# Optimization experiments

Hardware: AMD Instinct MI355X
Metric: run time of the kernel (lower is better)

The kernel has to match this reference:

```python
import jax, jax.numpy as jnp
import numpy as np

NUM_ITEMS = 50000
B = 512      # batch of (user, item) pairs
L = 50       # padded per-user item-list length
K = 20       # top_k: length of each context channel
H = 32       # hidden_dim
D = 32       # output_dim


def setup_inputs() -> dict:
    key = jax.random.key(0)
    ks = jax.random.split(key, 8)
    ctx = jax.random.normal(ks[0], (NUM_ITEMS, 10, K), dtype=jnp.float32)
    item_idxs = jax.random.randint(ks[1], (B,), 0, NUM_ITEMS)
    user_items = jax.random.randint(ks[2], (B, L), 0, NUM_ITEMS)
    user_lens = jax.random.randint(ks[3], (B,), 1, L + 1)  # ragged lengths in [1, L]
    W1 = jax.random.normal(ks[4], (5, 1, H), dtype=jnp.float32) * 0.1
    b1 = jnp.zeros((5, H), dtype=jnp.float32)
    W2 = jax.random.normal(ks[5], (5, H, D), dtype=jnp.float32) * 0.1
    b2 = jnp.zeros((5, D), dtype=jnp.float32)
    Wout = jax.random.normal(ks[6], (D, 1), dtype=jnp.float32) * 0.1
    bout = jnp.zeros((1,), dtype=jnp.float32)
    return dict(ctx=ctx, W1=W1, b1=b1, W2=W2, b2=b2, Wout=Wout, bout=bout,
                item_idxs=item_idxs, user_items=user_items, user_lens=user_lens)


def _item_rep(feat, W1, b1, W2, b2):
    """feat: [..., 10, K] context channels -> [..., 5*K, D] item representation.
    Channels (2c, 2c+1) go through com_{c+1}: a shared 1->H->D MLP applied to each
    scalar (unsqueeze(1) in the original), outputs of the two channels multiplied."""
    prefix = feat.shape[:-2]
    x = feat.reshape(prefix + (5, 2, K))                     # [..., 5, 2, K]
    w1 = W1[:, 0, :].reshape((5, 1, 1, H))                   # input_dim == 1
    h = jax.nn.relu(x[..., None] * w1 + b1.reshape((5, 1, 1, H)))   # [..., 5, 2, K, H]
    o = jnp.einsum('...cpkh,chd->...cpkd', h, W2) + b2.reshape((5, 1, 1, D))
    rep = o[..., 0, :, :] * o[..., 1, :, :]                  # [..., 5, K, D]
    return rep.reshape(prefix + (5 * K, D))


def reference(ctx, W1, b1, W2, b2, Wout, bout, item_idxs, user_items, user_lens):
    # Target-item representations: gather contexts then tiny MLPs. [B, 5K, D]
    item_rep = _item_rep(ctx[item_idxs], W1, b1, W2, b2)
    # Per-user item reps (padded ragged) and masked mean over the item list.
    u_rep = _item_rep(ctx[user_items], W1, b1, W2, b2)       # [B, L, 5K, D]
    mask = (jnp.arange(L)[None, :] < user_lens[:, None]).astype(u_rep.dtype)  # [B, L]
    u_mean = jnp.einsum('blnd,bl->bnd', u_rep, mask) / user_lens[:, None, None].astype(u_rep.dtype)
    inter = u_mean * item_rep                                # [B, 5K, D]
    pred = jax.nn.sigmoid(inter @ Wout + bout)               # [B, 5K, 1]
    return pred.reshape(B * 5 * K, 1)
```

## Files before the change

### kernel.cpp

```cpp
#include <hip/hip_runtime.h>
#include <math.h>

#define NITEMS 50000
#define BATCH  512
#define LLEN   50
#define KTOP   20
#define HDIM   32
#define DDIM   32
#define NCH    5
#define NSEG   33
#define NSCAL  200
#define NCELL  100
#define THRP   33
#define NWAVE  8

#define WS_THRS  0
#define WS_AB    (NCH*HDIM)
#define WS_ORDER 10720

__global__ __launch_bounds__(256) void cnn_setup(
        const float* __restrict__ W1, const float* __restrict__ b1,
        const float* __restrict__ W2, const float* __restrict__ b2,
        const int* __restrict__ user_lens,
        float* __restrict__ ws, int* __restrict__ order) {
    const int tid = threadIdx.x;

    if (blockIdx.x < NSEG) {
        __shared__ float sW1[NCH*HDIM], sB1[NCH*HDIM], sThr[NCH*HDIM];
        __shared__ int   sRank[NCH*HDIM];
        __shared__ float sW2[NCH*HDIM*DDIM];
        __shared__ float sB2[NCH*DDIM];

        for (int i = tid; i < NCH*HDIM; i += 256) { sW1[i] = W1[i]; sB1[i] = b1[i]; }
        for (int i = tid; i < NCH*HDIM*DDIM; i += 256) sW2[i] = W2[i];
        for (int i = tid; i < NCH*DDIM; i += 256) sB2[i] = b2[i];
        __syncthreads();

        for (int i = tid; i < NCH*HDIM; i += 256) {
            float w = sW1[i];
            sThr[i] = (w != 0.f) ? (-sB1[i] / w) : INFINITY;
        }
        __syncthreads();

        for (int i = tid; i < NCH*HDIM; i += 256) {
            int c = i / HDIM, h = i % HDIM;
            float thr = sThr[i];
            int rank = 0;
            for (int h2 = 0; h2 < HDIM; ++h2) {
                float thr2 = sThr[c*HDIM + h2];
                rank += (thr2 < thr || (thr2 == thr && h2 < h)) ? 1 : 0;
            }
            sRank[i] = rank;
            if (blockIdx.x == 0) ws[WS_THRS + c*HDIM + rank] = thr;
        }
        __syncthreads();

        const int s = blockIdx.x;
        if (tid < NCH*DDIM) {
            int c = tid / DDIM, d = tid % DDIM;
            float A = 0.f, Bv = 0.f;
#pragma unroll
            for (int h = 0; h < HDIM; ++h) {
                float w  = sW1[c*HDIM + h];
                float bb = sB1[c*HDIM + h];
                int   r  = sRank[c*HDIM + h];
                bool active = (w > 0.f) ? (r < s) : ((w < 0.f) ? (r >= s) : (bb > 0.f));
                if (active) {
                    float w2 = sW2[(c*HDIM + h)*DDIM + d];
                    A  = fmaf(w,  w2, A);
                    Bv = fmaf(bb, w2, Bv);
                }
            }
            Bv += sB2[c*DDIM + d];
            float* AB = ws + WS_AB;
            AB[((c*NSEG + s)*DDIM + d)*2 + 0] = A;
            AB[((c*NSEG + s)*DDIM + d)*2 + 1] = Bv;
        }
    } else {
        __shared__ int k512[BATCH], v512[BATCH];
        for (int i = tid; i < BATCH; i += 256) { k512[i] = user_lens[i]; v512[i] = i; }
        __syncthreads();
        for (int k = 2; k <= BATCH; k <<= 1) {
            for (int j = k >> 1; j > 0; j >>= 1) {
                int i   = ((tid & ~(j - 1)) << 1) | (tid & (j - 1));
                int ixj = i | j;
                bool up = ((i & k) == 0);
                int ka = k512[i], kb = k512[ixj];
                if ((ka > kb) == up) {
                    k512[i] = kb; k512[ixj] = ka;
                    int va = v512[i]; v512[i] = v512[ixj]; v512[ixj] = va;
                }
                __syncthreads();
            }
        }
        for (int i = tid; i < BATCH; i += 256) order[i] = v512[i];
    }
}

__global__ __launch_bounds__(512, 4) void cnn_main(
        const float* __restrict__ ctx,  const float* __restrict__ ws,
        const float* __restrict__ Wout, const float* __restrict__ bout,
        const int* __restrict__ item_idxs, const int* __restrict__ user_items,
        const int* __restrict__ user_lens, const int* __restrict__ order,
        float* __restrict__ out) {
    __shared__ float4 sAB4[NCH*NSEG*16];
    __shared__ float  sThrS[NCH*THRP];
    __shared__ float4 sxo[NWAVE][NCELL];
    __shared__ union WScr {
        float rawx[NSCAL];
        float pRed[NCELL];
    } wscr[NWAVE];

    const int tid  = threadIdx.x;
    const int w    = tid >> 6;
    const int lane = tid & 63;
    const int g    = (lane >> 4) & 3;
    const int d16  = lane & 15;

    const float4* ABg = reinterpret_cast<const float4*>(ws + WS_AB);
    for (int i = tid; i < NCH*NSEG*16; i += 512) sAB4[i] = ABg[i];
    for (int i = tid; i < NCH*THRP; i += 512) {
        int c = i / THRP, j = i - c*THRP;
        sThrS[i] = (j < HDIM) ? ws[WS_THRS + c*HDIM + j] : 0.f;
    }

    const int rank = (blockIdx.x < 256) ? blockIdx.x : (767 - blockIdx.x);
    const int b    = order[rank];
    const int len  = user_lens[b];
    const float inv_len = 1.f / (float)len;
    const float bo = bout[0];
    const float wa = Wout[2*d16], wb = Wout[2*d16 + 1];

    int sc[4], sdst[4];
#pragma unroll
    for (int r = 0; r < 4; ++r) {
        int idx  = lane + 64*r;
        int c    = idx / 40, rr = idx - c*40;
        sc[r]    = c;
        sdst[r]  = (c*KTOP + (rr % KTOP))*2 + (rr / KTOP);
    }

    const int nstripe = (len > w) ? ((len - w + NWAVE - 1) / NWAVE) : 0;
    const int nj = 1 + nstripe;

    float wta[25], wtb[25], acc[25];
#pragma unroll
    for (int i = 0; i < 25; ++i) acc[i] = 0.f;

    __syncthreads();

    float4 x4 = make_float4(0.f, 0.f, 0.f, 0.f);
    {
        int it0 = item_idxs[b];
        if (lane < 50) x4 = *((const float4*)(ctx + (size_t)it0*NSCAL) + lane);
    }

    float2* sxoF2 = reinterpret_cast<float2*>(&sxo[w][0]);
    for (int j = 0; j < nj; ++j) {
        if (lane < 50) *((float4*)&wscr[w].rawx[0] + lane) = x4;
        __builtin_amdgcn_wave_barrier();

        float4 xn4 = make_float4(0.f, 0.f, 0.f, 0.f);
        if (j + 1 < nj) {
            int nit = user_items[b*LLEN + w + NWAVE*j];
            if (lane < 50) xn4 = *((const float4*)(ctx + (size_t)nit*NSCAL) + lane);
        }

#pragma unroll
        for (int r = 0; r < 4; ++r) {
            int idx = lane + 64*r;
            if (idx < NSCAL) {
                float xv = wscr[w].rawx[idx];
                int base = sc[r]*THRP;
                int pos = 0;
                pos += (sThrS[base + pos + 15] < xv) ? 16 : 0;
                pos += (sThrS[base + pos + 7]  < xv) ? 8  : 0;
                pos += (sThrS[base + pos + 3]  < xv) ? 4  : 0;
                pos += (sThrS[base + pos + 1]  < xv) ? 2  : 0;
                pos += (sThrS[base + pos]      < xv) ? 1  : 0;
                int off = (sc[r]*NSEG + pos) << 8;
                sxoF2[sdst[r]] = make_float2(xv, __int_as_float(off));
            }
        }
        __builtin_amdgcn_wave_barrier();

        if (j == 0) {
#pragma unroll
            for (int i = 0; i < 25; ++i) {
                float4 xo = sxo[w][i*4 + g];
                const float4* p0 = (const float4*)((const char*)sAB4 + __float_as_int(xo.y)) + d16;
                const float4* p1 = (const float4*)((const char*)sAB4 + __float_as_int(xo.w)) + d16;
                float4 ab0 = *p0, ab1 = *p1;
                wta[i] = fmaf(xo.x, ab0.x, ab0.y) * fmaf(xo.z, ab1.x, ab1.y) * wa;
                wtb[i] = fmaf(xo.x, ab0.z, ab0.w) * fmaf(xo.z, ab1.z, ab1.w) * wb;
            }
        } else {
#pragma unroll
            for (int i = 0; i < 25; ++i) {
                float4 xo = sxo[w][i*4 + g];
                const float4* p0 = (const float4*)((const char*)sAB4 + __float_as_int(xo.y)) + d16;
                const float4* p1 = (const float4*)((const char*)sAB4 + __float_as_int(xo.w)) + d16;
                float4 ab0 = *p0, ab1 = *p1;
                float ra = fmaf(xo.x, ab0.x, ab0.y) * fmaf(xo.z, ab1.x, ab1.y);
                float rb = fmaf(xo.x, ab0.z, ab0.w) * fmaf(xo.z, ab1.z, ab1.w);
                acc[i] = fmaf(ra, wta[i], fmaf(rb, wtb[i], acc[i]));
            }
        }
        __builtin_amdgcn_wave_barrier();
        x4 = xn4;
    }

#pragma unroll
    for (int i = 0; i < 25; ++i) {
        float v = acc[i];
        v += __shfl_xor(v, 1, 64);
        v += __shfl_xor(v, 2, 64);
        v += __shfl_xor(v, 4, 64);
        v += __shfl_xor(v, 8, 64);
        if (d16 == 0) wscr[w].pRed[i*4 + g] = v;
    }
    __syncthreads();
    if (tid < NCELL) {
        float p = 0.f;
#pragma unroll
        for (int q = 0; q < NWAVE; ++q) p += wscr[q].pRed[tid];
        out[b*NCELL + tid] = 1.f / (1.f + expf(-(p*inv_len + bo)));
    }
}

extern "C" void kernel_launch(void* const* d_in, const int* in_sizes, int n_in,
                              void* d_out, int out_size, void* d_ws, size_t ws_size,
                              hipStream_t stream) {
    const float* ctx   = (const float*)d_in[0];
    const float* W1    = (const float*)d_in[1];
    const float* b1    = (const float*)d_in[2];
    const float* W2    = (const float*)d_in[3];
    const float* b2    = (const float*)d_in[4];
    const float* Wout  = (const float*)d_in[5];
    const float* bout  = (const float*)d_in[6];
    const int* item_idxs  = (const int*)d_in[7];
    const int* user_items = (const int*)d_in[8];
    const int* user_lens  = (const int*)d_in[9];
    float* out = (float*)d_out;
    float* ws  = (float*)d_ws;
    int*   order = (int*)(ws + WS_ORDER);

    cnn_setup<<<NSEG + 1, 256, 0, stream>>>(W1, b1, W2, b2, user_lens, ws, order);
    cnn_main<<<BATCH, 512, 0, stream>>>(ctx, ws, Wout, bout,
                                        item_idxs, user_items, user_lens,
                                        order, out);
}
```

Baseline: 130.6 us.

## Store per-segment affine MLP coefficients in fp16 and use packed half math

The precomputed piecewise-linear A/B coefficients are now stored as fp16 pairs, which halves their shared-memory footprint. The main loop computes the two channel outputs with packed half2 FMAs and accumulates through fdot2. The lane layout changes from 16 lanes × 2 dims per cell to 8 lanes × 4 dims, which cuts the per-lane cell slots from 25 to 13 and drops one shuffle stage in the reduction. The aim is fewer ALU and LDS instructions per cell, at the cost of fp16 rounding in the representations and weights, which could affect accuracy.

```diff
diff --git a/kernel.cpp b/kernel.cpp
--- a/kernel.cpp
+++ b/kernel.cpp
@@ -13,10 +13,22 @@
 #define NCELL  100
 #define THRP   33
 #define NWAVE  8
+#define CSLOT  13
+
+typedef _Float16 h2 __attribute__((ext_vector_type(2)));
+
+static __device__ __forceinline__ float dot2_acc(h2 a, h2 b, float c) {
+#if __has_builtin(__builtin_amdgcn_fdot2)
+    return __builtin_amdgcn_fdot2(a, b, c, false);
+#else
+    return fmaf((float)a.x, (float)b.x, fmaf((float)a.y, (float)b.y, c));
+#endif
+}
 
 #define WS_THRS  0
-#define WS_AB    (NCH*HDIM)
-#define WS_ORDER 10720
+#define WS_AB16  160
+#define WS_ORDER 5440
+
 
 __global__ __launch_bounds__(256) void cnn_setup(
         const float* __restrict__ W1, const float* __restrict__ b1,
@@ -46,9 +58,9 @@
             int c = i / HDIM, h = i % HDIM;
             float thr = sThr[i];
             int rank = 0;
-            for (int h2 = 0; h2 < HDIM; ++h2) {
-                float thr2 = sThr[c*HDIM + h2];
-                rank += (thr2 < thr || (thr2 == thr && h2 < h)) ? 1 : 0;
+            for (int h2i = 0; h2i < HDIM; ++h2i) {
+                float thr2 = sThr[c*HDIM + h2i];
+                rank += (thr2 < thr || (thr2 == thr && h2i < h)) ? 1 : 0;
             }
             sRank[i] = rank;
             if (blockIdx.x == 0) ws[WS_THRS + c*HDIM + rank] = thr;
@@ -72,9 +84,12 @@
                 }
             }
             Bv += sB2[c*DDIM + d];
-            float* AB = ws + WS_AB;
-            AB[((c*NSEG + s)*DDIM + d)*2 + 0] = A;
-            AB[((c*NSEG + s)*DDIM + d)*2 + 1] = Bv;
+            unsigned short* ab = (unsigned short*)(ws + WS_AB16);
+            int d4 = d >> 2, dd = d & 3;
+            int base = ((c*NSEG + s)*32 + d4*4)*2;
+            _Float16 ah = (_Float16)A, bh = (_Float16)Bv;
+            ab[base + 4*(dd>>1) + (dd&1)]     = __builtin_bit_cast(unsigned short, ah);
+            ab[base + 4*(dd>>1) + 2 + (dd&1)] = __builtin_bit_cast(unsigned short, bh);
         }
     } else {
         __shared__ int k512[BATCH], v512[BATCH];
@@ -103,7 +118,7 @@
         const int* __restrict__ item_idxs, const int* __restrict__ user_items,
         const int* __restrict__ user_lens, const int* __restrict__ order,
         float* __restrict__ out) {
-    __shared__ float4 sAB4[NCH*NSEG*16];
+    __shared__ unsigned int sAB16[NCH*NSEG*32];
     __shared__ float  sThrS[NCH*THRP];
     __shared__ float4 sxo[NWAVE][NCELL];
     __shared__ union WScr {
@@ -114,11 +129,12 @@
     const int tid  = threadIdx.x;
     const int w    = tid >> 6;
     const int lane = tid & 63;
-    const int g    = (lane >> 4) & 3;
-    const int d16  = lane & 15;
-
-    const float4* ABg = reinterpret_cast<const float4*>(ws + WS_AB);
-    for (int i = tid; i < NCH*NSEG*16; i += 512) sAB4[i] = ABg[i];
+    const int g    = lane >> 3;
+    const int d4   = lane & 7;
+
+    const uint4* ABg = reinterpret_cast<const uint4*>(ws + WS_AB16);
+    uint4* sAB4 = reinterpret_cast<uint4*>(sAB16);
+    for (int i = tid; i < NCH*NSEG*8; i += 512) sAB4[i] = ABg[i];
     for (int i = tid; i < NCH*THRP; i += 512) {
         int c = i / THRP, j = i - c*THRP;
         sThrS[i] = (j < HDIM) ? ws[WS_THRS + c*HDIM + j] : 0.f;
@@ -129,23 +145,28 @@
     const int len  = user_lens[b];
     const float inv_len = 1.f / (float)len;
     const float bo = bout[0];
-    const float wa = Wout[2*d16], wb = Wout[2*d16 + 1];
-
-    int sc[4], sdst[4];
+    const float w0 = Wout[4*d4], w1 = Wout[4*d4+1],
+                w2 = Wout[4*d4+2], w3 = Wout[4*d4+3];
+
+    int sc[4], sdx[4], sdo[4];
 #pragma unroll
     for (int r = 0; r < 4; ++r) {
         int idx  = lane + 64*r;
         int c    = idx / 40, rr = idx - c*40;
-        sc[r]    = c;
-        sdst[r]  = (c*KTOP + (rr % KTOP))*2 + (rr / KTOP);
+        int cell = c*KTOP + (rr % KTOP);
+        int p    = rr / KTOP;
+        sc[r]  = c;
+        sdx[r] = cell*16 + p*4;
+        sdo[r] = cell*16 + 8 + p*2;
     }
 
     const int nstripe = (len > w) ? ((len - w + NWAVE - 1) / NWAVE) : 0;
     const int nj = 1 + nstripe;
 
-    float wta[25], wtb[25], acc[25];
-#pragma unroll
-    for (int i = 0; i < 25; ++i) acc[i] = 0.f;
+    h2    wtA[CSLOT], wtB[CSLOT];
+    float acc[CSLOT];
+#pragma unroll
+    for (int i = 0; i < CSLOT; ++i) acc[i] = 0.f;
 
     __syncthreads();
 
@@ -155,7 +176,7 @@
         if (lane < 50) x4 = *((const float4*)(ctx + (size_t)it0*NSCAL) + lane);
     }
 
-    float2* sxoF2 = reinterpret_cast<float2*>(&sxo[w][0]);
+    char* sxoB = (char*)&sxo[w][0];
     for (int j = 0; j < nj; ++j) {
         if (lane < 50) *((float4*)&wscr[w].rawx[0] + lane) = x4;
         __builtin_amdgcn_wave_barrier();
@@ -178,32 +199,38 @@
                 pos += (sThrS[base + pos + 3]  < xv) ? 4  : 0;
                 pos += (sThrS[base + pos + 1]  < xv) ? 2  : 0;
                 pos += (sThrS[base + pos]      < xv) ? 1  : 0;
-                int off = (sc[r]*NSEG + pos) << 8;
-                sxoF2[sdst[r]] = make_float2(xv, __int_as_float(off));
+                int off = (sc[r]*NSEG + pos) << 7;
+                *(float*)(sxoB + sdx[r]) = xv;
+                *(unsigned short*)(sxoB + sdo[r]) = (unsigned short)off;
             }
         }
         __builtin_amdgcn_wave_barrier();
 
-        if (j == 0) {
-#pragma unroll
-            for (int i = 0; i < 25; ++i) {
-                float4 xo = sxo[w][i*4 + g];
-                const float4* p0 = (const float4*)((const char*)sAB4 + __float_as_int(xo.y)) + d16;
-                const float4* p1 = (const float4*)((const char*)sAB4 + __float_as_int(xo.w)) + d16;
-                float4 ab0 = *p0, ab1 = *p1;
-                wta[i] = fmaf(xo.x, ab0.x, ab0.y) * fmaf(xo.z, ab1.x, ab1.y) * wa;
-                wtb[i] = fmaf(xo.x, ab0.z, ab0.w) * fmaf(xo.z, ab1.z, ab1.w) * wb;
-            }
-        } else {
-#pragma unroll
-            for (int i = 0; i < 25; ++i) {
-                float4 xo = sxo[w][i*4 + g];
-                const float4* p0 = (const float4*)((const char*)sAB4 + __float_as_int(xo.y)) + d16;
-                const float4* p1 = (const float4*)((const char*)sAB4 + __float_as_int(xo.w)) + d16;
-                float4 ab0 = *p0, ab1 = *p1;
-                float ra = fmaf(xo.x, ab0.x, ab0.y) * fmaf(xo.z, ab1.x, ab1.y);
-                float rb = fmaf(xo.x, ab0.z, ab0.w) * fmaf(xo.z, ab1.z, ab1.w);
-                acc[i] = fmaf(ra, wta[i], fmaf(rb, wtb[i], acc[i]));
+#pragma unroll
+        for (int i = 0; i < CSLOT; ++i) {
+            int cell = g + 8*i;
+            if (cell < NCELL) {
+                float4 xo = sxo[w][cell];
+                unsigned int offs = __builtin_bit_cast(unsigned int, xo.z);
+                const uint4* p0 = (const uint4*)((const char*)sAB16 + (offs & 0xffffu) + (d4 << 4));
+                const uint4* p1 = (const uint4*)((const char*)sAB16 + (offs >> 16)     + (d4 << 4));
+                uint4 q0 = *p0, q1 = *p1;
+                _Float16 x0h = (_Float16)xo.x, x1h = (_Float16)xo.y;
+                h2 x0 = {x0h, x0h}, x1 = {x1h, x1h};
+                h2 o0a = x0 * __builtin_bit_cast(h2, q0.x) + __builtin_bit_cast(h2, q0.y);
+                h2 o0b = x0 * __builtin_bit_cast(h2, q0.z) + __builtin_bit_cast(h2, q0.w);
+                h2 o1a = x1 * __builtin_bit_cast(h2, q1.x) + __builtin_bit_cast(h2, q1.y);
+                h2 o1b = x1 * __builtin_bit_cast(h2, q1.z) + __builtin_bit_cast(h2, q1.w);
+                h2 repa = o0a * o1a;
+                h2 repb = o0b * o1b;
+                if (j == 0) {
+                    wtA[i] = h2{(_Float16)((float)repa.x * w0),
+                                (_Float16)((float)repa.y * w1)};
+                    wtB[i] = h2{(_Float16)((float)repb.x * w2),
+                                (_Float16)((float)repb.y * w3)};
+                } else {
+                    acc[i] = dot2_acc(repa, wtA[i], dot2_acc(repb, wtB[i], acc[i]));
+                }
             }
         }
         __builtin_amdgcn_wave_barrier();
@@ -211,13 +238,13 @@
     }
 
 #pragma unroll
-    for (int i = 0; i < 25; ++i) {
+    for (int i = 0; i < CSLOT; ++i) {
+        int cell = g + 8*i;
         float v = acc[i];
         v += __shfl_xor(v, 1, 64);
         v += __shfl_xor(v, 2, 64);
         v += __shfl_xor(v, 4, 64);
-        v += __shfl_xor(v, 8, 64);
-        if (d16 == 0) wscr[w].pRed[i*4 + g] = v;
+        if (d4 == 0 && cell < NCELL) wscr[w].pRed[cell] = v;
     }
     __syncthreads();
     if (tid < NCELL) {
```

Result: slower. 135.0 us (+3.4%).
